# Kernel tuning notes

Hardware: AMD Instinct MI355X
Metric: run time of the kernel (lower is better)

## Reference

```python
import jax, jax.numpy as jnp
import numpy as np

DIM = 1024
N_HEADS = 16
HEAD_DIM = DIM // N_HEADS
SCALE = 1.0 / HEAD_DIM ** 0.5


def setup_inputs() -> dict:
    key = jax.random.key(0)
    k1, k2, k3, k4, k5 = jax.random.split(key, 5)
    B, T = 4, 2048
    x = jax.random.normal(k1, (B, T, DIM), dtype=jnp.float32)
    # torch nn.Linear weights: y = x @ W.T + b
    w_qkv = jax.random.normal(k2, (3 * DIM, DIM), dtype=jnp.float32) * 0.02
    b_qkv = jax.random.normal(k3, (3 * DIM,), dtype=jnp.float32) * 0.02
    w_proj = jax.random.normal(k4, (DIM, DIM), dtype=jnp.float32) * 0.02
    b_proj = jax.random.normal(k5, (DIM,), dtype=jnp.float32) * 0.02
    return {"x": x, "w_qkv": w_qkv, "b_qkv": b_qkv, "w_proj": w_proj, "b_proj": b_proj}


def reference(x, w_qkv, b_qkv, w_proj, b_proj):
    B, T, D = x.shape
    qkv = x @ w_qkv.T + b_qkv                              # [B, T, 3D]
    qkv = qkv.reshape(B, T, 3, N_HEADS, HEAD_DIM)
    qkv = jnp.transpose(qkv, (2, 0, 3, 1, 4))              # [3, B, h, T, d]
    q, k, v = qkv[0], qkv[1], qkv[2]
    s = jnp.einsum('bhqd,bhkd->bhqk', q, k) * SCALE        # [B, h, T, T]
    attn = jax.nn.softmax(s, axis=-1)
    out = jnp.einsum('bhqk,bhkd->bqhd', attn, v)           # [B, T, h, d]
    out = out.reshape(B, T, D)
    return out @ w_proj.T + b_proj
```

## Files before the change

### kernel.cpp

```cpp
#include <hip/hip_runtime.h>
#include <stdint.h>

typedef short short8 __attribute__((ext_vector_type(8)));
typedef _Float16 half4 __attribute__((ext_vector_type(4)));
typedef _Float16 half8 __attribute__((ext_vector_type(8)));
typedef __fp16 fp16x2 __attribute__((ext_vector_type(2)));
typedef unsigned int uint2v __attribute__((ext_vector_type(2)));
typedef unsigned int uintx4 __attribute__((ext_vector_type(4)));
typedef float floatx4 __attribute__((ext_vector_type(4)));

#define LOG2E 1.44269504088896340736f
#define QSCALE (0.125f * LOG2E)

static __device__ __forceinline__ unsigned short f2bf(float f) {
  unsigned int u = __float_as_uint(f);
  u += 0x7fffu + ((u >> 16) & 1u);
  return (unsigned short)(u >> 16);
}

static __device__ __forceinline__ float fexp2(float x) {
#if __has_builtin(__builtin_amdgcn_exp2f)
  return __builtin_amdgcn_exp2f(x);
#else
  return exp2f(x);
#endif
}

#define GLD_LDS16(gp, lp)                                                      \
  __builtin_amdgcn_global_load_lds(                                            \
      (const __attribute__((address_space(1))) void*)(gp),                     \
      (__attribute__((address_space(3))) void*)(lp), 16, 0, 0)

__global__ __launch_bounds__(256) void cvt_f32_bf16(
    const float* __restrict__ in, unsigned short* __restrict__ out, int n) {
  int i = (blockIdx.x * 256 + threadIdx.x) * 4;
  if (i >= n) return;
  float4 v = *(const float4*)(in + i);
  ushort4 u;
  u.x = f2bf(v.x); u.y = f2bf(v.y); u.z = f2bf(v.z); u.w = f2bf(v.w);
  *(ushort4*)(out + i) = u;
}

template <int MODE>
__global__ __launch_bounds__(256, 4) void gemm_bt(
    const unsigned short* __restrict__ A, const unsigned short* __restrict__ Bm,
    const float* __restrict__ bias, float* __restrict__ outF,
    unsigned short* __restrict__ qo, unsigned short* __restrict__ ko,
    _Float16* __restrict__ vto, int M, int N, int K) {
  __shared__ unsigned short As[128 * 64];
  __shared__ unsigned short Bs[128 * 64];
  const int tid = threadIdx.x;
  const int w = tid >> 6, l = tid & 63;
  const int lr = l & 15, lg = l >> 4;
  const int nbn = N >> 7;
  const int nwg = gridDim.x;
  const int bid = blockIdx.x;
  const int cpx = nwg >> 3;
  const int swz = (bid & 7) * cpx + (bid >> 3);
  const int bm = swz / nbn, bn = swz % nbn;
  const int wm = w >> 1, wn = w & 1;

  floatx4 acc[4][4];
#pragma unroll
  for (int i = 0; i < 4; ++i)
#pragma unroll
    for (int j = 0; j < 4; ++j) acc[i][j] = (floatx4){0.f, 0.f, 0.f, 0.f};

  const int sw0 = ((0 * 4 + lg) ^ (lr & 7)) * 8;
  const int sw1 = ((1 * 4 + lg) ^ (lr & 7)) * 8;

  for (int k0 = 0; k0 < K; k0 += 64) {
#pragma unroll
    for (int i = 0; i < 4; ++i) {
      int c = i * 256 + tid;
      int row = c >> 3, sl = (c & 7) ^ (row & 7);
      const unsigned short* ga =
          A + ((size_t)bm * 128 + row) * K + k0 + sl * 8;
      GLD_LDS16(ga, As + (size_t)(i * 256 + w * 64) * 8);
    }
#pragma unroll
    for (int i = 0; i < 4; ++i) {
      int c = i * 256 + tid;
      int row = c >> 3, sl = (c & 7) ^ (row & 7);
      const unsigned short* gb =
          Bm + ((size_t)bn * 128 + row) * K + k0 + sl * 8;
      GLD_LDS16(gb, Bs + (size_t)(i * 256 + w * 64) * 8);
    }
    __syncthreads();
#pragma unroll
    for (int kk = 0; kk < 2; ++kk) {
      const int sw = kk ? sw1 : sw0;
      short8 af[4], bf[4];
#pragma unroll
      for (int i = 0; i < 4; ++i)
        af[i] = *(const short8*)&As[(wm * 64 + i * 16 + lr) * 64 + sw];
#pragma unroll
      for (int j = 0; j < 4; ++j)
        bf[j] = *(const short8*)&Bs[(wn * 64 + j * 16 + lr) * 64 + sw];
#pragma unroll
      for (int i = 0; i < 4; ++i)
#pragma unroll
        for (int j = 0; j < 4; ++j)
          acc[i][j] = __builtin_amdgcn_mfma_f32_16x16x32_bf16(af[i], bf[j],
                                                              acc[i][j], 0, 0, 0);
    }
    __syncthreads();
  }

#pragma unroll
  for (int i = 0; i < 4; ++i) {
    int row0 = bm * 128 + wm * 64 + i * 16 + lg * 4;
#pragma unroll
    for (int j = 0; j < 4; ++j) {
      int col = bn * 128 + wn * 64 + j * 16 + lr;
      float bv = bias[col];
#pragma unroll
      for (int jj = 0; jj < 4; ++jj) {
        float v = acc[i][j][jj] + bv;
        int r = row0 + jj;
        if (MODE == 0) {
          outF[(size_t)r * N + col] = v;
        } else {
          int three = col >> 10, cc = col & 1023;
          int h = cc >> 6, d = cc & 63;
          int b = r >> 11, t = r & 2047;
          if (three == 0)
            qo[(((size_t)(b * 16 + h)) * 2048 + t) * 64 + d] = f2bf(v * QSCALE);
          else if (three == 1)
            ko[(((size_t)(b * 16 + h)) * 2048 + t) * 64 + d] = f2bf(v);
          else
            vto[(((size_t)(b * 16 + h)) * 64 + d) * 2048 + t] = (_Float16)v;
        }
      }
    }
  }
}

__global__ __launch_bounds__(256, 3) void attn_fwd(
    const unsigned short* __restrict__ Qg, const unsigned short* __restrict__ Kg,
    const _Float16* __restrict__ VTg, unsigned short* __restrict__ Og) {
  __shared__ unsigned short Ks[2][64 * 64];
  __shared__ _Float16 Vs[2][64 * 64];

  const int bid0 = blockIdx.x;
  const int bid = (bid0 & 7) * 128 + (bid0 >> 3);
  const int bh = bid >> 4, qt = bid & 15;
  const int b = bh >> 4, hh = bh & 15;
  const int tid = threadIdx.x, w = tid >> 6, l = tid & 63;
  const int l4 = l & 15, g = l >> 4;
  const unsigned short* Q = Qg + (size_t)bh * (2048 * 64);
  const unsigned short* Kp = Kg + (size_t)bh * (2048 * 64);
  const _Float16* VT = VTg + (size_t)bh * (64 * 2048);
  const int qw = qt * 128 + w * 32;

  const int r0 = tid >> 3;
  const int s0 = (tid & 7) ^ (r0 & 7);
  const int kv0 = (r0 & 16) ? (((r0 & 15) >> 2) * 8 + 4 + (r0 & 3))
                            : ((r0 >> 2) * 8 + (r0 & 3));
  const unsigned short* kp0 = Kp + (size_t)kv0 * 64 + s0 * 8;
  const unsigned short* kp1 = Kp + (size_t)(kv0 + 32) * 64 + s0 * 8;
  const _Float16* vp0 = VT + (size_t)r0 * 2048 + s0 * 8;
  const _Float16* vp1 = VT + (size_t)(r0 + 32) * 2048 + s0 * 8;
  unsigned short* ksd0 = &Ks[0][tid * 8];
  unsigned short* ksd1 = &Ks[0][(256 + tid) * 8];
  _Float16* vsd0 = &Vs[0][tid * 8];
  _Float16* vsd1 = &Vs[0][(256 + tid) * 8];

#define STAGE(bufofs, tt)                                                     \
  do {                                                                        \
    GLD_LDS16(kp0 + (size_t)(tt) * 64, ksd0 + (bufofs) * 4096);               \
    GLD_LDS16(kp1 + (size_t)(tt) * 64, ksd1 + (bufofs) * 4096);               \
    GLD_LDS16(vp0 + (tt), vsd0 + (bufofs) * 4096);                            \
    GLD_LDS16(vp1 + (tt), vsd1 + (bufofs) * 4096);                            \
  } while (0)

  const int kb0 = l4 * 64 + ((g ^ (l4 & 7)) * 8);
  const int kb1 = l4 * 64 + (((4 + g) ^ (l4 & 7)) * 8);
  int vb[2];
#pragma unroll
  for (int B = 0; B < 2; ++B)
    vb[B] = l4 * 64 + (((B * 4 + g) ^ (l4 & 7)) * 8);

  short8 qf[2][2];
#pragma unroll
  for (int qs = 0; qs < 2; ++qs)
#pragma unroll
    for (int c = 0; c < 2; ++c)
      qf[qs][c] =
          *(const short8*)&Q[(size_t)(qw + qs * 16 + l4) * 64 + c * 32 + g * 8];

  half8 onesv;
#pragma unroll
  for (int e = 0; e < 8; ++e) onesv[e] = (_Float16)1.0f;

  floatx4 o[2][4];
#pragma unroll
  for (int qs = 0; qs < 2; ++qs)
#pragma unroll
    for (int db = 0; db < 4; ++db) o[qs][db] = (floatx4){0.f, 0.f, 0.f, 0.f};
  floatx4 osum[2] = {(floatx4){0.f, 0.f, 0.f, 0.f}, (floatx4){0.f, 0.f, 0.f, 0.f}};
  float m[2] = {0.f, 0.f};

  STAGE(0, 0);
  __syncthreads();

#pragma unroll 2
  for (int it = 0; it < 32; ++it) {
    const int cur = it & 1;
    if (it + 1 < 32) STAGE(cur ^ 1, (it + 1) * 64);

    floatx4 s[2][4];
    const floatx4 i0 = (floatx4){-m[0], -m[0], -m[0], -m[0]};
    const floatx4 i1 = (floatx4){-m[1], -m[1], -m[1], -m[1]};
    __builtin_amdgcn_s_setprio(1);
#pragma unroll
    for (int f = 0; f < 4; ++f) {
      short8 kf0 = *(const short8*)&Ks[cur][kb0 + f * 1024];
      short8 kf1 = *(const short8*)&Ks[cur][kb1 + f * 1024];
      floatx4 t00 = __builtin_amdgcn_mfma_f32_16x16x32_bf16(kf0, qf[0][0], i0, 0, 0, 0);
      s[0][f] = __builtin_amdgcn_mfma_f32_16x16x32_bf16(kf1, qf[0][1], t00, 0, 0, 0);
      floatx4 t10 = __builtin_amdgcn_mfma_f32_16x16x32_bf16(kf0, qf[1][0], i1, 0, 0, 0);
      s[1][f] = __builtin_amdgcn_mfma_f32_16x16x32_bf16(kf1, qf[1][1], t10, 0, 0, 0);
    }
    __builtin_amdgcn_s_setprio(0);

    uint2v pu[2][4];
#pragma unroll
    for (int qs = 0; qs < 2; ++qs) {
      float e[16];
#pragma unroll
      for (int f = 0; f < 4; ++f)
#pragma unroll
        for (int jj = 0; jj < 4; ++jj) e[f * 4 + jj] = fexp2(s[qs][f][jj]);

      float p01 = fmaxf(fmaxf(s[qs][0][0], s[qs][0][1]), fmaxf(s[qs][0][2], s[qs][0][3]));
      float p23 = fmaxf(fmaxf(s[qs][1][0], s[qs][1][1]), fmaxf(s[qs][1][2], s[qs][1][3]));
      float p45 = fmaxf(fmaxf(s[qs][2][0], s[qs][2][1]), fmaxf(s[qs][2][2], s[qs][2][3]));
      float p67 = fmaxf(fmaxf(s[qs][3][0], s[qs][3][1]), fmaxf(s[qs][3][2], s[qs][3][3]));
      float pp = fmaxf(fmaxf(p01, p23), fmaxf(p45, p67));

      if (!__all(pp <= 8.0f)) {
        float pm = fmaxf(pp, __shfl_xor(pp, 16));
        pm = fmaxf(pm, __shfl_xor(pm, 32));
        float dm = fmaxf(pm, 0.0f);
        m[qs] += dm;
        float al = fexp2(-dm);
#pragma unroll
        for (int jj = 0; jj < 4; ++jj) {
          float alr = __shfl(al, g * 4 + jj);
          o[qs][0][jj] *= alr; o[qs][1][jj] *= alr;
          o[qs][2][jj] *= alr; o[qs][3][jj] *= alr;
          osum[qs][jj] *= alr;
        }
#pragma unroll
        for (int f = 0; f < 4; ++f)
#pragma unroll
          for (int jj = 0; jj < 4; ++jj)
            e[f * 4 + jj] = fexp2(s[qs][f][jj] - dm);
      }

#pragma unroll
      for (int f = 0; f < 4; ++f) {
        fp16x2 plo = __builtin_amdgcn_cvt_pkrtz(e[f * 4 + 0], e[f * 4 + 1]);
        fp16x2 phi = __builtin_amdgcn_cvt_pkrtz(e[f * 4 + 2], e[f * 4 + 3]);
        pu[qs][f].x = __builtin_bit_cast(unsigned int, plo);
        pu[qs][f].y = __builtin_bit_cast(unsigned int, phi);
      }
    }

    __builtin_amdgcn_s_setprio(1);
#pragma unroll
    for (int B = 0; B < 2; ++B) {
      uintx4 ua0, ua1;
      ua0.x = pu[0][2 * B].x;     ua0.y = pu[0][2 * B].y;
      ua0.z = pu[0][2 * B + 1].x; ua0.w = pu[0][2 * B + 1].y;
      ua1.x = pu[1][2 * B].x;     ua1.y = pu[1][2 * B].y;
      ua1.z = pu[1][2 * B + 1].x; ua1.w = pu[1][2 * B + 1].y;
      half8 pa0 = __builtin_bit_cast(half8, ua0);
      half8 pa1 = __builtin_bit_cast(half8, ua1);
      osum[0] = __builtin_amdgcn_mfma_f32_16x16x32_f16(pa0, onesv, osum[0], 0, 0, 0);
      osum[1] = __builtin_amdgcn_mfma_f32_16x16x32_f16(pa1, onesv, osum[1], 0, 0, 0);
#pragma unroll
      for (int db = 0; db < 4; ++db) {
        half8 vf = *(const half8*)&Vs[cur][vb[B] + db * 1024];
        o[0][db] = __builtin_amdgcn_mfma_f32_16x16x32_f16(pa0, vf, o[0][db], 0, 0, 0);
        o[1][db] = __builtin_amdgcn_mfma_f32_16x16x32_f16(pa1, vf, o[1][db], 0, 0, 0);
      }
    }
    __builtin_amdgcn_s_setprio(0);
    __syncthreads();
  }

#pragma unroll
  for (int qs = 0; qs < 2; ++qs) {
    float inv[4];
#pragma unroll
    for (int jj = 0; jj < 4; ++jj) inv[jj] = 1.f / osum[qs][jj];
#pragma unroll
    for (int db = 0; db < 4; ++db)
#pragma unroll
      for (int jj = 0; jj < 4; ++jj)
        Og[((size_t)b * 2048 + qw + qs * 16 + g * 4 + jj) * 1024 + hh * 64 +
           db * 16 + l4] = f2bf(o[qs][db][jj] * inv[jj]);
  }
#undef STAGE
}

extern "C" void kernel_launch(void* const* d_in, const int* in_sizes, int n_in,
                              void* d_out, int out_size, void* d_ws, size_t ws_size,
                              hipStream_t stream) {
  const float* x = (const float*)d_in[0];
  const float* w_qkv = (const float*)d_in[1];
  const float* b_qkv = (const float*)d_in[2];
  const float* w_proj = (const float*)d_in[3];
  const float* b_proj = (const float*)d_in[4];
  float* out = (float*)d_out;

  char* p = (char*)d_ws;
  unsigned short* xb = (unsigned short*)p;     p += (size_t)8192 * 1024 * 2;
  unsigned short* wqkvb = (unsigned short*)p;  p += (size_t)3072 * 1024 * 2;
  unsigned short* wprojb = (unsigned short*)p; p += (size_t)1024 * 1024 * 2;
  unsigned short* qb = (unsigned short*)p;     p += (size_t)64 * 2048 * 64 * 2;
  unsigned short* kb = (unsigned short*)p;     p += (size_t)64 * 2048 * 64 * 2;
  _Float16* vtb = (_Float16*)p;                p += (size_t)64 * 64 * 2048 * 2;
  unsigned short* attnb = (unsigned short*)p;  p += (size_t)8192 * 1024 * 2;

  cvt_f32_bf16<<<dim3(8192), dim3(256), 0, stream>>>(x, xb, 8192 * 1024);
  cvt_f32_bf16<<<dim3(3072), dim3(256), 0, stream>>>(w_qkv, wqkvb, 3072 * 1024);
  cvt_f32_bf16<<<dim3(1024), dim3(256), 0, stream>>>(w_proj, wprojb, 1024 * 1024);

  gemm_bt<1><<<dim3(64 * 24), dim3(256), 0, stream>>>(
      xb, wqkvb, b_qkv, nullptr, qb, kb, vtb, 8192, 3072, 1024);

  attn_fwd<<<dim3(1024), dim3(256), 0, stream>>>(qb, kb, vtb, attnb);

  gemm_bt<0><<<dim3(64 * 8), dim3(256), 0, stream>>>(
      attnb, wprojb, b_proj, out, nullptr, nullptr, nullptr, 8192, 1024, 1024);
}
```

Baseline: 197.1 us.

## Add 256x256 double-buffered 8-wave QKV GEMM and fuse conversion kernels

Replaces the QKV projection GEMM with a new 512-thread kernel that uses 256x256 tiles, double-buffered LDS fed by direct global-to-LDS loads, XOR-swizzled layout and a four-phase schedule. Each phase interleaves LDS reads, the next tile's prefetch and raw barriers with MFMA under raised priority. The aim is to raise data reuse per tile and hide global-load latency behind compute. It also merges the three fp32-to-bf16 conversion launches into one kernel to cut launch overhead. The trade-off is one workgroup per CU with heavy register and LDS use, and only 384 workgroups.

```diff
diff --git a/kernel.cpp b/kernel.cpp
--- a/kernel.cpp
+++ b/kernel.cpp
@@ -31,10 +31,25 @@
       (const __attribute__((address_space(1))) void*)(gp),                     \
       (__attribute__((address_space(3))) void*)(lp), 16, 0, 0)
 
-__global__ __launch_bounds__(256) void cvt_f32_bf16(
-    const float* __restrict__ in, unsigned short* __restrict__ out, int n) {
-  int i = (blockIdx.x * 256 + threadIdx.x) * 4;
-  if (i >= n) return;
+#define FENCE() asm volatile("" ::: "memory")
+#define RAWBAR()                                                               \
+  do {                                                                         \
+    FENCE();                                                                   \
+    __builtin_amdgcn_s_barrier();                                              \
+    FENCE();                                                                   \
+  } while (0)
+
+__global__ __launch_bounds__(256) void cvt_all(
+    const float* __restrict__ x, unsigned short* __restrict__ xb,
+    const float* __restrict__ wqkv, unsigned short* __restrict__ wqkvb,
+    const float* __restrict__ wproj, unsigned short* __restrict__ wprojb) {
+  int bid = blockIdx.x;
+  const float* in;
+  unsigned short* out;
+  if (bid < 8192) { in = x; out = xb; }
+  else if (bid < 11264) { in = wqkv; out = wqkvb; bid -= 8192; }
+  else { in = wproj; out = wprojb; bid -= 11264; }
+  int i = (bid * 256 + threadIdx.x) * 4;
   float4 v = *(const float4*)(in + i);
   ushort4 u;
   u.x = f2bf(v.x); u.y = f2bf(v.y); u.z = f2bf(v.z); u.w = f2bf(v.w);
@@ -42,11 +57,134 @@
 }
 
 template <int MODE>
-__global__ __launch_bounds__(256, 4) void gemm_bt(
+__global__ __launch_bounds__(512, 1) void gemm8p(
     const unsigned short* __restrict__ A, const unsigned short* __restrict__ Bm,
     const float* __restrict__ bias, float* __restrict__ outF,
     unsigned short* __restrict__ qo, unsigned short* __restrict__ ko,
     _Float16* __restrict__ vto, int M, int N, int K) {
+  __shared__ unsigned short Asl[2][256 * 64];
+  __shared__ unsigned short Bsl[2][256 * 64];
+  const int tid = threadIdx.x;
+  const int wid = tid >> 6, l = tid & 63;
+  const int lr = l & 15, lg = l >> 4;
+  const int wm = wid >> 2, wn = wid & 3;
+  const int nbn = N >> 8;
+  const int nwg = gridDim.x, bid = blockIdx.x;
+  const int cpx = nwg >> 3;
+  const int swz = (bid & 7) * cpx + (bid >> 3);
+  const int bm = swz / nbn, bn = swz % nbn;
+  const int KT = K >> 6;
+
+  const int srow = tid >> 3;
+  const int ssl = (tid & 7) ^ (srow & 7);
+  const unsigned short* Asrc = A + ((size_t)bm * 256 + srow) * K + ssl * 8;
+  const unsigned short* Bsrc = Bm + ((size_t)bn * 256 + srow) * K + ssl * 8;
+
+#define BURST(slot, kt)                                                        \
+  do {                                                                         \
+    _Pragma("unroll")                                                          \
+    for (int h = 0; h < 2; ++h)                                                \
+      _Pragma("unroll")                                                        \
+      for (int u = 0; u < 2; ++u) {                                            \
+        GLD_LDS16(Asrc + (size_t)(h * 128 + u * 64) * K + (kt) * 64,           \
+                  &Asl[slot][h * 8192 + u * 4096 + tid * 8]);                  \
+        GLD_LDS16(Bsrc + (size_t)(h * 128 + u * 64) * K + (kt) * 64,           \
+                  &Bsl[slot][h * 8192 + u * 4096 + tid * 8]);                  \
+      }                                                                        \
+  } while (0)
+
+  const int swk0 = ((0 * 4 + lg) ^ (lr & 7)) * 8;
+  const int swk1 = ((1 * 4 + lg) ^ (lr & 7)) * 8;
+  const int arb = (wm * 128 + lr) * 64;
+  const int brb = (wn * 64 + lr) * 64;
+
+  floatx4 acc[8][4];
+#pragma unroll
+  for (int i = 0; i < 8; ++i)
+#pragma unroll
+    for (int j = 0; j < 4; ++j) acc[i][j] = (floatx4){0.f, 0.f, 0.f, 0.f};
+
+#define PHASE(SL, RH, CH, DOBURST, BKT, BSLOT, DOVM)                           \
+  do {                                                                         \
+    short8 av[4][2], bv[2][2];                                                 \
+    _Pragma("unroll")                                                          \
+    for (int ii = 0; ii < 4; ++ii) {                                           \
+      av[ii][0] = *(const short8*)&Asl[SL][arb + (RH * 64 + ii * 16) * 64 + swk0]; \
+      av[ii][1] = *(const short8*)&Asl[SL][arb + (RH * 64 + ii * 16) * 64 + swk1]; \
+    }                                                                          \
+    _Pragma("unroll")                                                          \
+    for (int jj = 0; jj < 2; ++jj) {                                           \
+      bv[jj][0] = *(const short8*)&Bsl[SL][brb + (CH * 32 + jj * 16) * 64 + swk0]; \
+      bv[jj][1] = *(const short8*)&Bsl[SL][brb + (CH * 32 + jj * 16) * 64 + swk1]; \
+    }                                                                          \
+    if (DOBURST) BURST(BSLOT, BKT);                                            \
+    RAWBAR();                                                                  \
+    __builtin_amdgcn_s_setprio(1);                                             \
+    _Pragma("unroll")                                                          \
+    for (int ii = 0; ii < 4; ++ii)                                             \
+      _Pragma("unroll")                                                        \
+      for (int jj = 0; jj < 2; ++jj) {                                         \
+        floatx4 tmp = __builtin_amdgcn_mfma_f32_16x16x32_bf16(                 \
+            av[ii][0], bv[jj][0], acc[RH * 4 + ii][CH * 2 + jj], 0, 0, 0);     \
+        acc[RH * 4 + ii][CH * 2 + jj] = __builtin_amdgcn_mfma_f32_16x16x32_bf16( \
+            av[ii][1], bv[jj][1], tmp, 0, 0, 0);                               \
+      }                                                                        \
+    __builtin_amdgcn_s_setprio(0);                                             \
+    if (DOVM) asm volatile("s_waitcnt vmcnt(0)" ::: "memory");                 \
+    RAWBAR();                                                                  \
+  } while (0)
+
+  BURST(0, 0);
+  asm volatile("s_waitcnt vmcnt(0)" ::: "memory");
+  RAWBAR();
+
+  for (int t = 0; t < (KT >> 1); ++t) {
+    const int k0 = 2 * t;
+    PHASE(0, 0, 0, true, k0 + 1, 1, false);
+    PHASE(0, 1, 0, false, 0, 0, false);
+    PHASE(0, 0, 1, false, 0, 0, false);
+    PHASE(0, 1, 1, false, 0, 0, true);
+    const bool more = (k0 + 2) < KT;
+    PHASE(1, 0, 0, more, k0 + 2, 0, false);
+    PHASE(1, 1, 0, false, 0, 0, false);
+    PHASE(1, 0, 1, false, 0, 0, false);
+    PHASE(1, 1, 1, false, 0, 0, true);
+  }
+
+#pragma unroll
+  for (int i = 0; i < 8; ++i) {
+    int row0 = bm * 256 + wm * 128 + i * 16 + lg * 4;
+#pragma unroll
+    for (int j = 0; j < 4; ++j) {
+      int col = bn * 256 + wn * 64 + j * 16 + lr;
+      float bv = bias[col];
+#pragma unroll
+      for (int jj = 0; jj < 4; ++jj) {
+        float v = acc[i][j][jj] + bv;
+        int r = row0 + jj;
+        if (MODE == 0) {
+          outF[(size_t)r * N + col] = v;
+        } else {
+          int three = col >> 10, cc = col & 1023;
+          int h = cc >> 6, d = cc & 63;
+          int b = r >> 11, tt = r & 2047;
+          if (three == 0)
+            qo[(((size_t)(b * 16 + h)) * 2048 + tt) * 64 + d] = f2bf(v * QSCALE);
+          else if (three == 1)
+            ko[(((size_t)(b * 16 + h)) * 2048 + tt) * 64 + d] = f2bf(v);
+          else
+            vto[(((size_t)(b * 16 + h)) * 64 + d) * 2048 + tt] = (_Float16)v;
+        }
+      }
+    }
+  }
+#undef PHASE
+#undef BURST
+}
+
+__global__ __launch_bounds__(256, 4) void gemm_bt(
+    const unsigned short* __restrict__ A, const unsigned short* __restrict__ Bm,
+    const float* __restrict__ bias, float* __restrict__ outF, int M, int N, int K) {
   __shared__ unsigned short As[128 * 64];
   __shared__ unsigned short Bs[128 * 64];
   const int tid = threadIdx.x;
@@ -115,23 +253,8 @@
       int col = bn * 128 + wn * 64 + j * 16 + lr;
       float bv = bias[col];
 #pragma unroll
-      for (int jj = 0; jj < 4; ++jj) {
-        float v = acc[i][j][jj] + bv;
-        int r = row0 + jj;
-        if (MODE == 0) {
-          outF[(size_t)r * N + col] = v;
-        } else {
-          int three = col >> 10, cc = col & 1023;
-          int h = cc >> 6, d = cc & 63;
-          int b = r >> 11, t = r & 2047;
-          if (three == 0)
-            qo[(((size_t)(b * 16 + h)) * 2048 + t) * 64 + d] = f2bf(v * QSCALE);
-          else if (three == 1)
-            ko[(((size_t)(b * 16 + h)) * 2048 + t) * 64 + d] = f2bf(v);
-          else
-            vto[(((size_t)(b * 16 + h)) * 64 + d) * 2048 + t] = (_Float16)v;
-        }
-      }
+      for (int jj = 0; jj < 4; ++jj)
+        outF[(size_t)(row0 + jj) * N + col] = acc[i][j][jj] + bv;
     }
   }
 }
@@ -325,15 +448,13 @@
   _Float16* vtb = (_Float16*)p;                p += (size_t)64 * 64 * 2048 * 2;
   unsigned short* attnb = (unsigned short*)p;  p += (size_t)8192 * 1024 * 2;
 
-  cvt_f32_bf16<<<dim3(8192), dim3(256), 0, stream>>>(x, xb, 8192 * 1024);
-  cvt_f32_bf16<<<dim3(3072), dim3(256), 0, stream>>>(w_qkv, wqkvb, 3072 * 1024);
-  cvt_f32_bf16<<<dim3(1024), dim3(256), 0, stream>>>(w_proj, wprojb, 1024 * 1024);
-
-  gemm_bt<1><<<dim3(64 * 24), dim3(256), 0, stream>>>(
+  cvt_all<<<dim3(12288), dim3(256), 0, stream>>>(x, xb, w_qkv, wqkvb, w_proj, wprojb);
+
+  gemm8p<1><<<dim3(384), dim3(512), 0, stream>>>(
       xb, wqkvb, b_qkv, nullptr, qb, kb, vtb, 8192, 3072, 1024);
 
   attn_fwd<<<dim3(1024), dim3(256), 0, stream>>>(qb, kb, vtb, attnb);
 
-  gemm_bt<0><<<dim3(64 * 8), dim3(256), 0, stream>>>(
-      attnb, wprojb, b_proj, out, nullptr, nullptr, nullptr, 8192, 1024, 1024);
-}
+  gemm_bt<<<dim3(64 * 8), dim3(256), 0, stream>>>(
+      attnb, wprojb, b_proj, out, 8192, 1024, 1024);
+}
```

Measured after the change: 220.8 us. 1.12x slower.
